# Performance work log

Hardware: AMD Instinct MI355X
Metric: run time of the kernel (lower is better)

The kernel has to match this reference:

```python
import jax, jax.numpy as jnp
import numpy as np

B, N, D, H = 16, 512, 256, 8
DK = D // H
EPS = 1e-6
NEG_INF = 1e12
LAM_ATT, LAM_DIST, LAM_ADJ = 0.3, 0.3, 0.4


def setup_inputs() -> dict:
    key = jax.random.key(0)
    ks = jax.random.split(key, 16)
    inp = {
        "query": jax.random.normal(ks[0], (B, N, D), jnp.float32),
        "key": jax.random.normal(ks[1], (B, N, D), jnp.float32),
        "value": jax.random.normal(ks[2], (B, N, D), jnp.float32),
        "adj_matrix": jax.random.uniform(ks[3], (B, N, N), jnp.float32),
        "distances_matrix": jax.random.uniform(ks[4], (B, N, N), jnp.float32),
        "edges_att": jnp.zeros((1,), jnp.float32),
        "mask": jnp.ones((B, N), jnp.int32),
    }
    s = 1.0 / np.sqrt(D)
    # four Linear(d_model, d_model): Wq, Wk, Wv, Wo (+ biases)
    for i, nm in enumerate(["q", "k", "v", "o"]):
        inp[f"W{nm}"] = jax.random.normal(ks[5 + 2 * i], (D, D), jnp.float32) * s
        inp[f"b{nm}"] = jax.random.normal(ks[6 + 2 * i], (D,), jnp.float32) * s
    return inp


def _proj(x, W, b):
    # [B,N,D] -> [B,H,N,DK]
    y = x @ W.T + b
    return y.reshape(B, N, H, DK).transpose(0, 2, 1, 3)


def reference(query, key, value, adj_matrix, distances_matrix, edges_att, mask,
              Wq, bq, Wk, bk, Wv, bv, Wo, bo):
    q = _proj(query, Wq, bq)
    k = _proj(key, Wk, bk)
    v = _proj(value, Wv, bv)

    valid = mask != 0  # [B,N] key-side validity

    # distance kernel: softmax(-d) over keys, masked positions -> 0 prob
    d_scores = jnp.where(valid[:, None, :], -distances_matrix, -jnp.inf)
    p_dist = jax.nn.softmax(d_scores, axis=-1)  # [B,N,N]

    # scaled dot-product attention with key mask
    scores = jnp.einsum("bhqd,bhkd->bhqk", q, k) / np.sqrt(DK)
    scores = jnp.where(valid[:, None, None, :], scores, -NEG_INF)
    p_attn = jax.nn.softmax(scores, axis=-1)  # [B,H,N,N]

    # row-normalized adjacency
    p_adj = adj_matrix / (adj_matrix.sum(axis=-1, keepdims=True) + EPS)  # [B,N,N]

    # blend three attention terms (broadcast dist/adj over heads)
    p_weighted = (LAM_ATT * p_attn
                  + LAM_DIST * p_dist[:, None]
                  + LAM_ADJ * p_adj[:, None])  # [B,H,N,N]

    x = jnp.einsum("bhqk,bhkd->bhqd", p_weighted, v)  # [B,H,N,DK]
    x = x.transpose(0, 2, 1, 3).reshape(B, N, D)
    out = x @ Wo.T + bo  # output projection (4th linear)
    return out
```

## Files before the change

kernel.cpp:

```cpp
#include <hip/hip_runtime.h>
#include <cstdint>
#include <cstddef>

#define B_  16
#define N_  512
#define D_  256
#define H_  8
#define DK_ 32

#define QKV_ELEMS 2097152

__device__ __align__(16) unsigned short g_Qb[QKV_ELEMS];
__device__ __align__(16) unsigned short g_Kb[QKV_ELEMS];
__device__ __align__(16) unsigned short g_VT[QKV_ELEMS];
__device__ __align__(16) unsigned short g_WoB[D_*D_];
__device__ __align__(16) unsigned short g_ST[B_*N_*N_];

typedef short v8s __attribute__((ext_vector_type(8)));
typedef float v4f __attribute__((ext_vector_type(4)));

__device__ __forceinline__ unsigned short f2b(float f){
  unsigned int x;
  __builtin_memcpy(&x, &f, 4);
  x = x + 0x7FFFu + ((x >> 16) & 1u);
  return (unsigned short)(x >> 16);
}
__device__ __forceinline__ v8s pack8(const float4 a, const float4 b){
  v8s o;
  o[0]=(short)f2b(a.x); o[1]=(short)f2b(a.y); o[2]=(short)f2b(a.z); o[3]=(short)f2b(a.w);
  o[4]=(short)f2b(b.x); o[5]=(short)f2b(b.y); o[6]=(short)f2b(b.z); o[7]=(short)f2b(b.w);
  return o;
}

__global__ __launch_bounds__(256) void fused_pre(
    const float* __restrict__ query, const float* __restrict__ key_,
    const float* __restrict__ value,
    const float* __restrict__ Wq, const float* __restrict__ bq,
    const float* __restrict__ Wk, const float* __restrict__ bk,
    const float* __restrict__ Wv, const float* __restrict__ bv,
    const float* __restrict__ Wo,
    const float* __restrict__ dist, const float* __restrict__ adjm,
    const int* __restrict__ mask)
{
  __shared__ unsigned short Wl[64*264];
  const int bid = blockIdx.x;
  const int t   = threadIdx.x;

  if (bid < 512){
    const int b   = bid & 15;
    const int qt  = bid >> 4;
    const int row = t >> 4;
    const int seg = t & 15;
    const size_t roff = ((size_t)(b*N_ + qt*16 + row))*N_ + seg*32;
    const float* dp = dist + roff;
    const float* ap = adjm + roff;
    const int*   mp = mask + b*N_ + seg*32;
    float ev[32], av[32];
    float lz = 0.f, la = 0.f;
    #pragma unroll
    for (int c = 0; c < 8; ++c){
      const float4 d4 = *reinterpret_cast<const float4*>(dp + c*4);
      const float4 a4 = *reinterpret_cast<const float4*>(ap + c*4);
      const int4   m4 = *reinterpret_cast<const int4*>(mp + c*4);
      ev[c*4+0] = m4.x ? __expf(-d4.x) : 0.f;
      ev[c*4+1] = m4.y ? __expf(-d4.y) : 0.f;
      ev[c*4+2] = m4.z ? __expf(-d4.z) : 0.f;
      ev[c*4+3] = m4.w ? __expf(-d4.w) : 0.f;
      av[c*4+0] = a4.x; av[c*4+1] = a4.y; av[c*4+2] = a4.z; av[c*4+3] = a4.w;
      lz += ev[c*4+0] + ev[c*4+1] + ev[c*4+2] + ev[c*4+3];
      la += a4.x + a4.y + a4.z + a4.w;
    }
    #pragma unroll
    for (int o = 1; o < 16; o <<= 1){
      lz += __shfl_xor(lz, o, 64);
      la += __shfl_xor(la, o, 64);
    }
    const float c0 = (lz > 0.f) ? 0.3f / lz : 0.f;
    const float c1 = 0.4f / (la + 1e-6f);
    unsigned short* dst = g_ST + roff;
    #pragma unroll
    for (int c2 = 0; c2 < 4; ++c2){
      v8s o8;
      #pragma unroll
      for (int i = 0; i < 8; ++i)
        o8[i] = (short)f2b(ev[c2*8+i]*c0 + av[c2*8+i]*c1);
      *reinterpret_cast<v8s*>(dst + c2*8) = o8;
    }
    return;
  }

  if (bid >= 2048){
    const int i = ((bid - 2048)*256 + t)*4;
    const float4 u = *reinterpret_cast<const float4*>(Wo + i);
    const int n = i >> 8, k = i & 255;
    ushort4 o4;
    o4.x = f2b(u.x); o4.y = f2b(u.y); o4.z = f2b(u.z); o4.w = f2b(u.w);
    *reinterpret_cast<ushort4*>(g_WoB + (size_t)(k >> 5)*8192 + (size_t)n*32 + (k & 31)) = o4;
    return;
  }

  const int gb = bid - 512;
  const int z  = gb >> 9;
  const int rr = gb & 511;
  const int mt = rr >> 2, nt = rr & 3;
  const float* Ap = (z==0) ? query : (z==1) ? key_ : value;
  const float* Wp = (z==0) ? Wq : (z==1) ? Wk : Wv;
  const float* bp = (z==0) ? bq : (z==1) ? bk : bv;
  const int w = t >> 6, lane = t & 63, kl = lane & 15, quad = lane >> 4;
  const int m0 = mt*64 + w*16;
  const int n0 = nt*64;

  {
    const int row = t >> 2;
    const int ks  = (t & 3) * 64;
    const float* src = Wp + (size_t)(n0+row)*256 + ks;
    unsigned short* dst = Wl + row*264 + ks;
    #pragma unroll
    for (int u = 0; u < 8; ++u){
      const float4 u0 = reinterpret_cast<const float4*>(src)[2*u];
      const float4 u1 = reinterpret_cast<const float4*>(src)[2*u+1];
      *reinterpret_cast<v8s*>(dst + u*8) = pack8(u0, u1);
    }
  }
  __syncthreads();

  v4f acc[4];
  #pragma unroll
  for (int nb = 0; nb < 4; ++nb) acc[nb] = (v4f){0.f,0.f,0.f,0.f};
  const int arow = m0 + kl;

  if (z == 2){
    #pragma unroll
    for (int k0 = 0; k0 < 256; k0 += 32){
      const float* ap = Ap + (size_t)arow*256 + k0 + quad*8;
      const v8s af = pack8(reinterpret_cast<const float4*>(ap)[0],
                           reinterpret_cast<const float4*>(ap)[1]);
      #pragma unroll
      for (int nb = 0; nb < 4; ++nb){
        const v8s wf = *reinterpret_cast<const v8s*>(&Wl[(nb*16+kl)*264 + k0 + quad*8]);
        acc[nb] = __builtin_amdgcn_mfma_f32_16x16x32_bf16(wf, af, acc[nb], 0, 0, 0);
      }
    }
    const int tok = m0 + kl, bb = tok >> 9, nr = tok & 511;
    #pragma unroll
    for (int nb = 0; nb < 4; ++nb)
      #pragma unroll
      for (int r = 0; r < 4; ++r){
        const int n = n0 + nb*16 + quad*4 + r;
        const float v = acc[nb][r] + bp[n];
        g_VT[(((size_t)bb*H_ + (n>>5))*16 + (nr>>5))*1024 + (size_t)(n&31)*32 + (nr&31)] = f2b(v);
      }
  } else {
    #pragma unroll
    for (int k0 = 0; k0 < 256; k0 += 32){
      const float* ap = Ap + (size_t)arow*256 + k0 + quad*8;
      const v8s af = pack8(reinterpret_cast<const float4*>(ap)[0],
                           reinterpret_cast<const float4*>(ap)[1]);
      #pragma unroll
      for (int nb = 0; nb < 4; ++nb){
        const v8s wf = *reinterpret_cast<const v8s*>(&Wl[(nb*16+kl)*264 + k0 + quad*8]);
        acc[nb] = __builtin_amdgcn_mfma_f32_16x16x32_bf16(af, wf, acc[nb], 0, 0, 0);
      }
    }
    unsigned short* dst = z ? g_Kb : g_Qb;
    #pragma unroll
    for (int nb = 0; nb < 4; ++nb){
      const int n = n0 + nb*16 + kl;
      const float bias = bp[n];
      #pragma unroll
      for (int r = 0; r < 4; ++r){
        const int m = m0 + quad*4 + r;
        const float v = acc[nb][r] + bias;
        dst[(((size_t)(m>>9)*H_ + (n>>5))*N_ + (m&511))*DK_ + (n&31)] = f2b(v);
      }
    }
  }
}

__global__ __launch_bounds__(512, 4) void attn_kernel(
    const int* __restrict__ mask, const float* __restrict__ bo,
    float* __restrict__ out)
{
  __shared__ unsigned short STl[16*520];
  __shared__ unsigned short Pl[8*16*40];
  __shared__ unsigned short Xl[16*272];
  const int bid = blockIdx.x;
  const int b  = bid & 15;
  const int qt = bid >> 4;
  const int q0 = qt*16;
  const int t  = threadIdx.x;
  const int w  = t >> 6, lane = t & 63;
  const int kl = lane & 15, quad = lane >> 4;

  {
    const int row = t >> 5;
    const int c16 = (t & 31) * 16;
    const unsigned short* src = g_ST + ((size_t)(b*N_ + q0 + row))*N_ + c16;
    *reinterpret_cast<v8s*>(&STl[row*520 + c16])     = *reinterpret_cast<const v8s*>(src);
    *reinterpret_cast<v8s*>(&STl[row*520 + c16 + 8]) = *reinterpret_cast<const v8s*>(src + 8);
  }

  const int h = w;
  const size_t bh = (size_t)b*H_ + h;
  const float scale = 0.17677669529663687f;
  const unsigned short* Qp = g_Qb + (bh*N_ + q0)*DK_;
  const unsigned short* Kp = g_Kb + bh*N_*DK_;
  const unsigned short* Vp = g_VT + bh*(size_t)(N_*DK_);
  unsigned short* Plw = Pl + w*640;
  const int* mrow = mask + b*N_;
  const v8s aq = *reinterpret_cast<const v8s*>(Qp + (size_t)kl*DK_ + quad*8);
  const v4f vz = {0.f, 0.f, 0.f, 0.f};

  v4f oA0 = vz, oA1 = vz;
  v4f oS0 = vz, oS1 = vz;
  float lsum[4] = {0.f, 0.f, 0.f, 0.f};

  __syncthreads();

  #pragma unroll 1
  for (int ch = 0; ch < 4; ++ch){
    const int k0 = ch*128;
    v4f acc[8];
    #pragma unroll
    for (int kb = 0; kb < 8; ++kb){
      const v8s bk = *reinterpret_cast<const v8s*>(Kp + (size_t)(k0 + kb*16 + kl)*DK_ + quad*8);
      acc[kb] = __builtin_amdgcn_mfma_f32_16x16x32_bf16(aq, bk, vz, 0, 0, 0);
    }
    #pragma unroll
    for (int kb = 0; kb < 8; ++kb){
      const bool valid = (mrow[k0 + kb*16 + kl] != 0);
      #pragma unroll
      for (int r = 0; r < 4; ++r){
        const float e = valid ? __expf(acc[kb][r]*scale) : 0.f;
        acc[kb][r] = e;
        lsum[r] += e;
      }
    }
    #pragma unroll
    for (int cc = 0; cc < 4; ++cc){
      #pragma unroll
      for (int r = 0; r < 4; ++r){
        Plw[(quad*4 + r)*40 + kl]      = f2b(acc[2*cc    ][r]);
        Plw[(quad*4 + r)*40 + 16 + kl] = f2b(acc[2*cc + 1][r]);
      }
      const int kk = k0 + cc*32;
      const v8s bp  = *reinterpret_cast<const v8s*>(&Plw[kl*40 + quad*8]);
      const v8s bst = *reinterpret_cast<const v8s*>(&STl[kl*520 + kk + quad*8]);
      const v8s av0 = *reinterpret_cast<const v8s*>(Vp + (size_t)(kk + kl)*32 + quad*8);
      const v8s av1 = *reinterpret_cast<const v8s*>(Vp + (size_t)(kk + 16 + kl)*32 + quad*8);
      oA0 = __builtin_amdgcn_mfma_f32_16x16x32_bf16(av0, bp,  oA0, 0, 0, 0);
      oS0 = __builtin_amdgcn_mfma_f32_16x16x32_bf16(av0, bst, oS0, 0, 0, 0);
      oA1 = __builtin_amdgcn_mfma_f32_16x16x32_bf16(av1, bp,  oA1, 0, 0, 0);
      oS1 = __builtin_amdgcn_mfma_f32_16x16x32_bf16(av1, bst, oS1, 0, 0, 0);
    }
  }

  #pragma unroll
  for (int r = 0; r < 4; ++r)
    #pragma unroll
    for (int o = 1; o < 16; o <<= 1) lsum[r] += __shfl_xor(lsum[r], o, 64);
  const float s01 = (kl & 1) ? lsum[1] : lsum[0];
  const float s23 = (kl & 1) ? lsum[3] : lsum[2];
  const float sv  = (kl & 2) ? s23 : s01;
  float inv = __shfl(sv, ((kl >> 2) << 4) | (kl & 3), 64);
  inv = (inv > 0.f) ? 0.3f / inv : 0.f;

  unsigned short* xr = Xl + kl*272 + h*32;
  #pragma unroll
  for (int r = 0; r < 4; ++r){
    xr[     quad*4 + r] = f2b(oA0[r]*inv + oS0[r]);
    xr[16 + quad*4 + r] = f2b(oA1[r]*inv + oS1[r]);
  }
  __syncthreads();

  {
    const int n0 = w*32;
    v4f a2[2];
    a2[0] = vz; a2[1] = vz;
    #pragma unroll
    for (int k0 = 0; k0 < 256; k0 += 32){
      const v8s af = *reinterpret_cast<const v8s*>(&Xl[kl*272 + k0 + quad*8]);
      #pragma unroll
      for (int nb = 0; nb < 2; ++nb){
        const v8s wf = *reinterpret_cast<const v8s*>(
            g_WoB + (size_t)(k0 >> 5)*8192 + (size_t)(n0 + nb*16 + kl)*32 + quad*8);
        a2[nb] = __builtin_amdgcn_mfma_f32_16x16x32_bf16(af, wf, a2[nb], 0, 0, 0);
      }
    }
    #pragma unroll
    for (int nb = 0; nb < 2; ++nb){
      const int n = n0 + nb*16 + kl;
      const float bias = bo[n];
      #pragma unroll
      for (int r = 0; r < 4; ++r)
        out[((size_t)(b*N_ + q0 + quad*4 + r))*256 + n] = a2[nb][r] + bias;
    }
  }
}

extern "C" void kernel_launch(void* const* d_in, const int* in_sizes, int n_in,
                              void* d_out, int out_size, void* d_ws, size_t ws_size,
                              hipStream_t stream)
{
  const float* query = (const float*)d_in[0];
  const float* key_  = (const float*)d_in[1];
  const float* value = (const float*)d_in[2];
  const float* adjm  = (const float*)d_in[3];
  const float* dist  = (const float*)d_in[4];
  const int*   mask  = (const int*)d_in[6];
  const float* Wq = (const float*)d_in[7];  const float* bq = (const float*)d_in[8];
  const float* Wk = (const float*)d_in[9];  const float* bk = (const float*)d_in[10];
  const float* Wv = (const float*)d_in[11]; const float* bv = (const float*)d_in[12];
  const float* Wo = (const float*)d_in[13]; const float* bo = (const float*)d_in[14];

  fused_pre<<<2112, 256, 0, stream>>>(query, key_, value,
                                      Wq, bq, Wk, bk, Wv, bv, Wo,
                                      dist, adjm, mask);
  attn_kernel<<<512, 512, 0, stream>>>(mask, bo, (float*)d_out);
}
```

Baseline: 180.4 us.

## Pre-convert weights to bf16 and fuse QKV projection with ST build per tile

Weight-to-bf16 conversion for Wq/Wk/Wv/Wo moves into a small separate kernel, so the QKV projection reads bf16 weights straight from global memory instead of restaging fp32 weights into LDS in every block. Each 512-thread block now builds the blended dist/adj tile for 16 query rows and also computes the Q, K and V projections for those same 16 tokens, with each wave owning one head. Operand order is swapped so Q/K and V outputs come out as vectorized ushort4 stores. The cost is an extra kernel launch and only 512 blocks doing the projection work, which may lower parallelism.

```diff
diff --git a/kernel.cpp b/kernel.cpp
--- a/kernel.cpp
+++ b/kernel.cpp
@@ -13,6 +13,9 @@
 __device__ __align__(16) unsigned short g_Qb[QKV_ELEMS];
 __device__ __align__(16) unsigned short g_Kb[QKV_ELEMS];
 __device__ __align__(16) unsigned short g_VT[QKV_ELEMS];
+__device__ __align__(16) unsigned short g_WqB[D_*D_];
+__device__ __align__(16) unsigned short g_WkB[D_*D_];
+__device__ __align__(16) unsigned short g_WvB[D_*D_];
 __device__ __align__(16) unsigned short g_WoB[D_*D_];
 __device__ __align__(16) unsigned short g_ST[B_*N_*N_];
 
@@ -32,33 +35,48 @@
   return o;
 }
 
-__global__ __launch_bounds__(256) void fused_pre(
+__global__ __launch_bounds__(256) void prep_w(
+    const float* __restrict__ Wq, const float* __restrict__ Wk,
+    const float* __restrict__ Wv, const float* __restrict__ Wo)
+{
+  const int bid = blockIdx.x;
+  const int z = bid >> 6;
+  const int i = ((bid & 63)*256 + (int)threadIdx.x)*4;
+  const float* src = (z==0)?Wq:(z==1)?Wk:(z==2)?Wv:Wo;
+  const float4 u = *reinterpret_cast<const float4*>(src + i);
+  ushort4 o4;
+  o4.x = f2b(u.x); o4.y = f2b(u.y); o4.z = f2b(u.z); o4.w = f2b(u.w);
+  if (z < 3){
+    unsigned short* dst = (z==0)?g_WqB:(z==1)?g_WkB:g_WvB;
+    *reinterpret_cast<ushort4*>(dst + i) = o4;
+  } else {
+    const int n = i >> 8, k = i & 255;
+    *reinterpret_cast<ushort4*>(g_WoB + ((size_t)(k >> 5))*8192 + (size_t)n*32 + (k & 31)) = o4;
+  }
+}
+
+__global__ __launch_bounds__(512) void qkv_st_kernel(
     const float* __restrict__ query, const float* __restrict__ key_,
-    const float* __restrict__ value,
-    const float* __restrict__ Wq, const float* __restrict__ bq,
-    const float* __restrict__ Wk, const float* __restrict__ bk,
-    const float* __restrict__ Wv, const float* __restrict__ bv,
-    const float* __restrict__ Wo,
-    const float* __restrict__ dist, const float* __restrict__ adjm,
-    const int* __restrict__ mask)
-{
-  __shared__ unsigned short Wl[64*264];
+    const float* __restrict__ value, const float* __restrict__ dist,
+    const float* __restrict__ adjm,  const int* __restrict__ mask,
+    const float* __restrict__ bq, const float* __restrict__ bk,
+    const float* __restrict__ bv)
+{
   const int bid = blockIdx.x;
-  const int t   = threadIdx.x;
-
-  if (bid < 512){
-    const int b   = bid & 15;
-    const int qt  = bid >> 4;
-    const int row = t >> 4;
-    const int seg = t & 15;
-    const size_t roff = ((size_t)(b*N_ + qt*16 + row))*N_ + seg*32;
+  const int b = bid & 15, qt = bid >> 4, q0 = qt*16;
+  const int t = threadIdx.x;
+  const int w = t >> 6, lane = t & 63, kl = lane & 15, quad = lane >> 4;
+
+  {
+    const int row = t >> 5, seg = t & 31;
+    const size_t roff = ((size_t)(b*N_ + q0 + row))*N_ + seg*16;
     const float* dp = dist + roff;
     const float* ap = adjm + roff;
-    const int*   mp = mask + b*N_ + seg*32;
-    float ev[32], av[32];
+    const int*   mp = mask + b*N_ + seg*16;
+    float ev[16], av[16];
     float lz = 0.f, la = 0.f;
     #pragma unroll
-    for (int c = 0; c < 8; ++c){
+    for (int c = 0; c < 4; ++c){
       const float4 d4 = *reinterpret_cast<const float4*>(dp + c*4);
       const float4 a4 = *reinterpret_cast<const float4*>(ap + c*4);
       const int4   m4 = *reinterpret_cast<const int4*>(mp + c*4);
@@ -66,112 +84,73 @@
       ev[c*4+1] = m4.y ? __expf(-d4.y) : 0.f;
       ev[c*4+2] = m4.z ? __expf(-d4.z) : 0.f;
       ev[c*4+3] = m4.w ? __expf(-d4.w) : 0.f;
-      av[c*4+0] = a4.x; av[c*4+1] = a4.y; av[c*4+2] = a4.z; av[c*4+3] = a4.w;
-      lz += ev[c*4+0] + ev[c*4+1] + ev[c*4+2] + ev[c*4+3];
-      la += a4.x + a4.y + a4.z + a4.w;
-    }
-    #pragma unroll
-    for (int o = 1; o < 16; o <<= 1){
+      av[c*4+0]=a4.x; av[c*4+1]=a4.y; av[c*4+2]=a4.z; av[c*4+3]=a4.w;
+      lz += ev[c*4+0]+ev[c*4+1]+ev[c*4+2]+ev[c*4+3];
+      la += a4.x+a4.y+a4.z+a4.w;
+    }
+    #pragma unroll
+    for (int o = 1; o < 32; o <<= 1){
       lz += __shfl_xor(lz, o, 64);
       la += __shfl_xor(la, o, 64);
     }
     const float c0 = (lz > 0.f) ? 0.3f / lz : 0.f;
     const float c1 = 0.4f / (la + 1e-6f);
-    unsigned short* dst = g_ST + roff;
-    #pragma unroll
-    for (int c2 = 0; c2 < 4; ++c2){
-      v8s o8;
-      #pragma unroll
-      for (int i = 0; i < 8; ++i)
-        o8[i] = (short)f2b(ev[c2*8+i]*c0 + av[c2*8+i]*c1);
-      *reinterpret_cast<v8s*>(dst + c2*8) = o8;
-    }
-    return;
-  }
-
-  if (bid >= 2048){
-    const int i = ((bid - 2048)*256 + t)*4;
-    const float4 u = *reinterpret_cast<const float4*>(Wo + i);
-    const int n = i >> 8, k = i & 255;
-    ushort4 o4;
-    o4.x = f2b(u.x); o4.y = f2b(u.y); o4.z = f2b(u.z); o4.w = f2b(u.w);
-    *reinterpret_cast<ushort4*>(g_WoB + (size_t)(k >> 5)*8192 + (size_t)n*32 + (k & 31)) = o4;
-    return;
-  }
-
-  const int gb = bid - 512;
-  const int z  = gb >> 9;
-  const int rr = gb & 511;
-  const int mt = rr >> 2, nt = rr & 3;
-  const float* Ap = (z==0) ? query : (z==1) ? key_ : value;
-  const float* Wp = (z==0) ? Wq : (z==1) ? Wk : Wv;
-  const float* bp = (z==0) ? bq : (z==1) ? bk : bv;
-  const int w = t >> 6, lane = t & 63, kl = lane & 15, quad = lane >> 4;
-  const int m0 = mt*64 + w*16;
-  const int n0 = nt*64;
-
-  {
-    const int row = t >> 2;
-    const int ks  = (t & 3) * 64;
-    const float* src = Wp + (size_t)(n0+row)*256 + ks;
-    unsigned short* dst = Wl + row*264 + ks;
-    #pragma unroll
-    for (int u = 0; u < 8; ++u){
-      const float4 u0 = reinterpret_cast<const float4*>(src)[2*u];
-      const float4 u1 = reinterpret_cast<const float4*>(src)[2*u+1];
-      *reinterpret_cast<v8s*>(dst + u*8) = pack8(u0, u1);
-    }
-  }
-  __syncthreads();
-
-  v4f acc[4];
-  #pragma unroll
-  for (int nb = 0; nb < 4; ++nb) acc[nb] = (v4f){0.f,0.f,0.f,0.f};
-  const int arow = m0 + kl;
-
-  if (z == 2){
-    #pragma unroll
-    for (int k0 = 0; k0 < 256; k0 += 32){
-      const float* ap = Ap + (size_t)arow*256 + k0 + quad*8;
-      const v8s af = pack8(reinterpret_cast<const float4*>(ap)[0],
-                           reinterpret_cast<const float4*>(ap)[1]);
-      #pragma unroll
-      for (int nb = 0; nb < 4; ++nb){
-        const v8s wf = *reinterpret_cast<const v8s*>(&Wl[(nb*16+kl)*264 + k0 + quad*8]);
-        acc[nb] = __builtin_amdgcn_mfma_f32_16x16x32_bf16(wf, af, acc[nb], 0, 0, 0);
-      }
-    }
-    const int tok = m0 + kl, bb = tok >> 9, nr = tok & 511;
-    #pragma unroll
-    for (int nb = 0; nb < 4; ++nb)
-      #pragma unroll
-      for (int r = 0; r < 4; ++r){
-        const int n = n0 + nb*16 + quad*4 + r;
-        const float v = acc[nb][r] + bp[n];
-        g_VT[(((size_t)bb*H_ + (n>>5))*16 + (nr>>5))*1024 + (size_t)(n&31)*32 + (nr&31)] = f2b(v);
-      }
-  } else {
-    #pragma unroll
-    for (int k0 = 0; k0 < 256; k0 += 32){
-      const float* ap = Ap + (size_t)arow*256 + k0 + quad*8;
-      const v8s af = pack8(reinterpret_cast<const float4*>(ap)[0],
-                           reinterpret_cast<const float4*>(ap)[1]);
-      #pragma unroll
-      for (int nb = 0; nb < 4; ++nb){
-        const v8s wf = *reinterpret_cast<const v8s*>(&Wl[(nb*16+kl)*264 + k0 + quad*8]);
-        acc[nb] = __builtin_amdgcn_mfma_f32_16x16x32_bf16(af, wf, acc[nb], 0, 0, 0);
-      }
-    }
-    unsigned short* dst = z ? g_Kb : g_Qb;
-    #pragma unroll
-    for (int nb = 0; nb < 4; ++nb){
-      const int n = n0 + nb*16 + kl;
-      const float bias = bp[n];
-      #pragma unroll
-      for (int r = 0; r < 4; ++r){
-        const int m = m0 + quad*4 + r;
-        const float v = acc[nb][r] + bias;
-        dst[(((size_t)(m>>9)*H_ + (n>>5))*N_ + (m&511))*DK_ + (n&31)] = f2b(v);
+    v8s s0, s1;
+    #pragma unroll
+    for (int i = 0; i < 8; ++i){
+      s0[i] = (short)f2b(ev[i]*c0   + av[i]*c1);
+      s1[i] = (short)f2b(ev[8+i]*c0 + av[8+i]*c1);
+    }
+    *reinterpret_cast<v8s*>(g_ST + roff)     = s0;
+    *reinterpret_cast<v8s*>(g_ST + roff + 8) = s1;
+  }
+
+  {
+    const size_t arow = ((size_t)(b*N_ + q0 + kl))*256;
+    const int n0 = w*32;
+    const v4f vz = {0.f,0.f,0.f,0.f};
+    #pragma unroll
+    for (int z = 0; z < 3; ++z){
+      const float* Ap = (z==0)?query:(z==1)?key_:value;
+      const unsigned short* WB = (z==0)?g_WqB:(z==1)?g_WkB:g_WvB;
+      const float* bp = (z==0)?bq:(z==1)?bk:bv;
+      v4f a0 = vz, a1 = vz;
+      #pragma unroll
+      for (int k0 = 0; k0 < 256; k0 += 32){
+        const float* app = Ap + arow + k0 + quad*8;
+        const v8s af = pack8(reinterpret_cast<const float4*>(app)[0],
+                             reinterpret_cast<const float4*>(app)[1]);
+        const v8s wf0 = *reinterpret_cast<const v8s*>(WB + ((size_t)(n0+kl))*256 + k0 + quad*8);
+        const v8s wf1 = *reinterpret_cast<const v8s*>(WB + ((size_t)(n0+16+kl))*256 + k0 + quad*8);
+        if (z < 2){
+          a0 = __builtin_amdgcn_mfma_f32_16x16x32_bf16(wf0, af, a0, 0, 0, 0);
+          a1 = __builtin_amdgcn_mfma_f32_16x16x32_bf16(wf1, af, a1, 0, 0, 0);
+        } else {
+          a0 = __builtin_amdgcn_mfma_f32_16x16x32_bf16(af, wf0, a0, 0, 0, 0);
+          a1 = __builtin_amdgcn_mfma_f32_16x16x32_bf16(af, wf1, a1, 0, 0, 0);
+        }
+      }
+      if (z < 2){
+        unsigned short* dst = (z==0) ? g_Qb : g_Kb;
+        #pragma unroll
+        for (int nb = 0; nb < 2; ++nb){
+          const v4f a = nb ? a1 : a0;
+          const int nn = n0 + nb*16 + quad*4;
+          const float4 b4 = *reinterpret_cast<const float4*>(bp + nn);
+          ushort4 o4;
+          o4.x=f2b(a[0]+b4.x); o4.y=f2b(a[1]+b4.y); o4.z=f2b(a[2]+b4.z); o4.w=f2b(a[3]+b4.w);
+          *reinterpret_cast<ushort4*>(dst + (((size_t)(b*H_+w))*N_ + q0 + kl)*DK_ + (nn & 31)) = o4;
+        }
+      } else {
+        #pragma unroll
+        for (int nb = 0; nb < 2; ++nb){
+          const v4f a = nb ? a1 : a0;
+          const float bias = bp[n0 + nb*16 + kl];
+          ushort4 o4;
+          o4.x=f2b(a[0]+bias); o4.y=f2b(a[1]+bias); o4.z=f2b(a[2]+bias); o4.w=f2b(a[3]+bias);
+          *reinterpret_cast<ushort4*>(g_VT + (((size_t)(b*H_+w))*16 + (qt>>1))*1024
+              + (size_t)(nb*16+kl)*32 + (qt&1)*16 + quad*4) = o4;
+        }
       }
     }
   }
@@ -313,8 +292,8 @@
   const float* Wv = (const float*)d_in[11]; const float* bv = (const float*)d_in[12];
   const float* Wo = (const float*)d_in[13]; const float* bo = (const float*)d_in[14];
 
-  fused_pre<<<2112, 256, 0, stream>>>(query, key_, value,
-                                      Wq, bq, Wk, bk, Wv, bv, Wo,
-                                      dist, adjm, mask);
+  prep_w<<<256, 256, 0, stream>>>(Wq, Wk, Wv, Wo);
+  qkv_st_kernel<<<512, 512, 0, stream>>>(query, key_, value, dist, adjm, mask,
+                                         bq, bk, bv);
   attn_kernel<<<512, 512, 0, stream>>>(mask, bo, (float*)d_out);
 }
```

New measurement: 190.1 us. 5.4% more time.

## Split fused prologue into weight-prep, blend-matrix and QKV GEMM kernels

Applied to the files above, without the earlier changes.

The single heterogeneous prologue kernel becomes three launches. A small kernel converts all four weight matrices to bf16 once. A separate kernel with 512 threads per block builds the blended distance/adjacency matrix using 16 elements per thread, where the old version used 32. The QKV GEMM then loads weights that are already in bf16, so each of its 1536 blocks no longer repeats the fp32-to-bf16 conversion. This removes redundant conversion work and divergent block roles, in exchange for extra launches and serialization between them.

```diff
diff --git a/kernel.cpp b/kernel.cpp
--- a/kernel.cpp
+++ b/kernel.cpp
@@ -13,6 +13,9 @@
 __device__ __align__(16) unsigned short g_Qb[QKV_ELEMS];
 __device__ __align__(16) unsigned short g_Kb[QKV_ELEMS];
 __device__ __align__(16) unsigned short g_VT[QKV_ELEMS];
+__device__ __align__(16) unsigned short g_WqB[D_*D_];
+__device__ __align__(16) unsigned short g_WkB[D_*D_];
+__device__ __align__(16) unsigned short g_WvB[D_*D_];
 __device__ __align__(16) unsigned short g_WoB[D_*D_];
 __device__ __align__(16) unsigned short g_ST[B_*N_*N_];
 
@@ -32,79 +35,96 @@
   return o;
 }
 
-__global__ __launch_bounds__(256) void fused_pre(
+__global__ __launch_bounds__(256) void prep_w(
+    const float* __restrict__ Wq, const float* __restrict__ Wk,
+    const float* __restrict__ Wv, const float* __restrict__ Wo)
+{
+  const int bid = blockIdx.x;
+  const int z = bid >> 6;
+  const int i = ((bid & 63)*256 + (int)threadIdx.x)*4;
+  const float* src = (z==0)?Wq:(z==1)?Wk:(z==2)?Wv:Wo;
+  const float4 u = *reinterpret_cast<const float4*>(src + i);
+  ushort4 o4;
+  o4.x = f2b(u.x); o4.y = f2b(u.y); o4.z = f2b(u.z); o4.w = f2b(u.w);
+  if (z < 3){
+    unsigned short* dst = (z==0)?g_WqB:(z==1)?g_WkB:g_WvB;
+    *reinterpret_cast<ushort4*>(dst + i) = o4;
+  } else {
+    const int n = i >> 8, k = i & 255;
+    *reinterpret_cast<ushort4*>(g_WoB + ((size_t)(k >> 5))*8192 + (size_t)n*32 + (k & 31)) = o4;
+  }
+}
+
+__global__ __launch_bounds__(512) void st_kernel(
+    const float* __restrict__ dist, const float* __restrict__ adjm,
+    const int* __restrict__ mask)
+{
+  const int bid = blockIdx.x;
+  const int b = bid & 15, qt = bid >> 4, q0 = qt*16;
+  const int t = threadIdx.x;
+  const int row = t >> 5, seg = t & 31;
+  const size_t roff = ((size_t)(b*N_ + q0 + row))*N_ + seg*16;
+  const float* dp = dist + roff;
+  const float* ap = adjm + roff;
+  const int*   mp = mask + b*N_ + seg*16;
+  const float4 d0 = reinterpret_cast<const float4*>(dp)[0];
+  const float4 d1 = reinterpret_cast<const float4*>(dp)[1];
+  const float4 d2 = reinterpret_cast<const float4*>(dp)[2];
+  const float4 d3 = reinterpret_cast<const float4*>(dp)[3];
+  const float4 a0 = reinterpret_cast<const float4*>(ap)[0];
+  const float4 a1 = reinterpret_cast<const float4*>(ap)[1];
+  const float4 a2 = reinterpret_cast<const float4*>(ap)[2];
+  const float4 a3 = reinterpret_cast<const float4*>(ap)[3];
+  const int4   m0 = reinterpret_cast<const int4*>(mp)[0];
+  const int4   m1 = reinterpret_cast<const int4*>(mp)[1];
+  const int4   m2 = reinterpret_cast<const int4*>(mp)[2];
+  const int4   m3 = reinterpret_cast<const int4*>(mp)[3];
+
+  float ev[16], av[16];
+  #define ST_STEP(i, d4, a4, m4) \
+    ev[i+0] = m4.x ? __expf(-d4.x) : 0.f;  av[i+0] = a4.x; \
+    ev[i+1] = m4.y ? __expf(-d4.y) : 0.f;  av[i+1] = a4.y; \
+    ev[i+2] = m4.z ? __expf(-d4.z) : 0.f;  av[i+2] = a4.z; \
+    ev[i+3] = m4.w ? __expf(-d4.w) : 0.f;  av[i+3] = a4.w;
+  ST_STEP(0,  d0, a0, m0)
+  ST_STEP(4,  d1, a1, m1)
+  ST_STEP(8,  d2, a2, m2)
+  ST_STEP(12, d3, a3, m3)
+  #undef ST_STEP
+  float lz = 0.f, la = 0.f;
+  #pragma unroll
+  for (int i = 0; i < 16; ++i){ lz += ev[i]; la += av[i]; }
+  #pragma unroll
+  for (int o = 1; o < 32; o <<= 1){
+    lz += __shfl_xor(lz, o, 64);
+    la += __shfl_xor(la, o, 64);
+  }
+  const float c0 = (lz > 0.f) ? 0.3f / lz : 0.f;
+  const float c1 = 0.4f / (la + 1e-6f);
+  v8s s0, s1;
+  #pragma unroll
+  for (int i = 0; i < 8; ++i){
+    s0[i] = (short)f2b(ev[i]*c0   + av[i]*c1);
+    s1[i] = (short)f2b(ev[8+i]*c0 + av[8+i]*c1);
+  }
+  *reinterpret_cast<v8s*>(g_ST + roff)     = s0;
+  *reinterpret_cast<v8s*>(g_ST + roff + 8) = s1;
+}
+
+__global__ __launch_bounds__(256) void qkv_gemm(
     const float* __restrict__ query, const float* __restrict__ key_,
     const float* __restrict__ value,
-    const float* __restrict__ Wq, const float* __restrict__ bq,
-    const float* __restrict__ Wk, const float* __restrict__ bk,
-    const float* __restrict__ Wv, const float* __restrict__ bv,
-    const float* __restrict__ Wo,
-    const float* __restrict__ dist, const float* __restrict__ adjm,
-    const int* __restrict__ mask)
+    const float* __restrict__ bq, const float* __restrict__ bk,
+    const float* __restrict__ bv)
 {
   __shared__ unsigned short Wl[64*264];
   const int bid = blockIdx.x;
   const int t   = threadIdx.x;
-
-  if (bid < 512){
-    const int b   = bid & 15;
-    const int qt  = bid >> 4;
-    const int row = t >> 4;
-    const int seg = t & 15;
-    const size_t roff = ((size_t)(b*N_ + qt*16 + row))*N_ + seg*32;
-    const float* dp = dist + roff;
-    const float* ap = adjm + roff;
-    const int*   mp = mask + b*N_ + seg*32;
-    float ev[32], av[32];
-    float lz = 0.f, la = 0.f;
-    #pragma unroll
-    for (int c = 0; c < 8; ++c){
-      const float4 d4 = *reinterpret_cast<const float4*>(dp + c*4);
-      const float4 a4 = *reinterpret_cast<const float4*>(ap + c*4);
-      const int4   m4 = *reinterpret_cast<const int4*>(mp + c*4);
-      ev[c*4+0] = m4.x ? __expf(-d4.x) : 0.f;
-      ev[c*4+1] = m4.y ? __expf(-d4.y) : 0.f;
-      ev[c*4+2] = m4.z ? __expf(-d4.z) : 0.f;
-      ev[c*4+3] = m4.w ? __expf(-d4.w) : 0.f;
-      av[c*4+0] = a4.x; av[c*4+1] = a4.y; av[c*4+2] = a4.z; av[c*4+3] = a4.w;
-      lz += ev[c*4+0] + ev[c*4+1] + ev[c*4+2] + ev[c*4+3];
-      la += a4.x + a4.y + a4.z + a4.w;
-    }
-    #pragma unroll
-    for (int o = 1; o < 16; o <<= 1){
-      lz += __shfl_xor(lz, o, 64);
-      la += __shfl_xor(la, o, 64);
-    }
-    const float c0 = (lz > 0.f) ? 0.3f / lz : 0.f;
-    const float c1 = 0.4f / (la + 1e-6f);
-    unsigned short* dst = g_ST + roff;
-    #pragma unroll
-    for (int c2 = 0; c2 < 4; ++c2){
-      v8s o8;
-      #pragma unroll
-      for (int i = 0; i < 8; ++i)
-        o8[i] = (short)f2b(ev[c2*8+i]*c0 + av[c2*8+i]*c1);
-      *reinterpret_cast<v8s*>(dst + c2*8) = o8;
-    }
-    return;
-  }
-
-  if (bid >= 2048){
-    const int i = ((bid - 2048)*256 + t)*4;
-    const float4 u = *reinterpret_cast<const float4*>(Wo + i);
-    const int n = i >> 8, k = i & 255;
-    ushort4 o4;
-    o4.x = f2b(u.x); o4.y = f2b(u.y); o4.z = f2b(u.z); o4.w = f2b(u.w);
-    *reinterpret_cast<ushort4*>(g_WoB + (size_t)(k >> 5)*8192 + (size_t)n*32 + (k & 31)) = o4;
-    return;
-  }
-
-  const int gb = bid - 512;
-  const int z  = gb >> 9;
-  const int rr = gb & 511;
+  const int z  = bid >> 9;
+  const int rr = bid & 511;
   const int mt = rr >> 2, nt = rr & 3;
   const float* Ap = (z==0) ? query : (z==1) ? key_ : value;
-  const float* Wp = (z==0) ? Wq : (z==1) ? Wk : Wv;
+  const unsigned short* WB = (z==0) ? g_WqB : (z==1) ? g_WkB : g_WvB;
   const float* bp = (z==0) ? bq : (z==1) ? bk : bv;
   const int w = t >> 6, lane = t & 63, kl = lane & 15, quad = lane >> 4;
   const int m0 = mt*64 + w*16;
@@ -113,14 +133,11 @@
   {
     const int row = t >> 2;
     const int ks  = (t & 3) * 64;
-    const float* src = Wp + (size_t)(n0+row)*256 + ks;
+    const unsigned short* src = WB + (size_t)(n0+row)*256 + ks;
     unsigned short* dst = Wl + row*264 + ks;
     #pragma unroll
-    for (int u = 0; u < 8; ++u){
-      const float4 u0 = reinterpret_cast<const float4*>(src)[2*u];
-      const float4 u1 = reinterpret_cast<const float4*>(src)[2*u+1];
-      *reinterpret_cast<v8s*>(dst + u*8) = pack8(u0, u1);
-    }
+    for (int u = 0; u < 8; ++u)
+      *reinterpret_cast<v8s*>(dst + u*8) = *reinterpret_cast<const v8s*>(src + u*8);
   }
   __syncthreads();
 
@@ -313,8 +330,8 @@
   const float* Wv = (const float*)d_in[11]; const float* bv = (const float*)d_in[12];
   const float* Wo = (const float*)d_in[13]; const float* bo = (const float*)d_in[14];
 
-  fused_pre<<<2112, 256, 0, stream>>>(query, key_, value,
-                                      Wq, bq, Wk, bk, Wv, bv, Wo,
-                                      dist, adjm, mask);
+  prep_w<<<256, 256, 0, stream>>>(Wq, Wk, Wv, Wo);
+  st_kernel<<<512, 512, 0, stream>>>(dist, adjm, mask);
+  qkv_gemm<<<1536, 256, 0, stream>>>(query, key_, value, bq, bk, bv);
   attn_kernel<<<512, 512, 0, stream>>>(mask, bo, (float*)d_out);
 }
```

Result: faster. 165.0 us (-8.5%).
